# Optimization experiments

Measured on AMD Instinct MI355X. Metric: run time of the kernel, lower is better.

## Reference

```python
import jax, jax.numpy as jnp
import numpy as np

N, I, D, K = 64, 8192, 128, 16


def setup_inputs() -> dict:
    key = jax.random.key(0)
    k1, k2 = jax.random.split(key)
    x = jax.random.normal(k1, (N, I, D), dtype=jnp.float32)
    # each point belongs to one of k clusters of its own batch element -> offset n*K
    ci = jax.random.randint(k2, (N, I), 0, K) + jnp.arange(N)[:, None] * K
    return {
        "feature_matrix_batch": x,
        "cluster_index": ci.reshape(-1).astype(jnp.int32),  # [N*I]
        "k": K,
    }


def reference(feature_matrix_batch, cluster_index, k):
    n, i, d = feature_matrix_batch.shape
    flat = feature_matrix_batch.reshape(-1, d)  # [N*I, D]
    # scatter_max over segment ids -> [N*k, D]
    out = jax.ops.segment_max(flat, cluster_index, num_segments=n * k)
    return out.reshape(n, k, d)
```

## Files before the change

kernel.cpp:

```cpp
#include <hip/hip_runtime.h>
#include <stdint.h>

#define NB 64
#define NI 8192
#define ND 128
#define NK 16
#define SEG (NK * ND)
#define OUT_ELEMS (NB * SEG)
#define MAPPED_NEG_INF 0x007FFFFFu

typedef float f4 __attribute__((ext_vector_type(4)));
typedef uint32_t u4 __attribute__((ext_vector_type(4)));

__device__ __forceinline__ uint32_t map_f32(float f) {
    uint32_t b = __float_as_uint(f);
    return b ^ ((uint32_t)((int32_t)b >> 31) | 0x80000000u);
}
__device__ __forceinline__ uint32_t unmap_u32(uint32_t m) {
    return (m & 0x80000000u) ? (m ^ 0x80000000u) : ~m;
}

template <int PPB>
__global__ __launch_bounds__(256, 8) void seg_partial(
        const float* __restrict__ x,
        const int* __restrict__ ci,
        uint32_t* __restrict__ ws) {
    constexpr int BPB = NI / PPB;
    __shared__ uint32_t loc[SEG];
    __shared__ int cidx[PPB];

    const int t = threadIdx.x;
    const int b = blockIdx.x;
    const int batch = b / BPB;
    const int row0 = batch * NI + (b % BPB) * PPB;

    for (int i = t; i < SEG; i += 256) loc[i] = MAPPED_NEG_INF;
    if (t < PPB / 4) {
        int4 c = ((const int4*)(ci + row0))[t];
        const int base = batch * NK;
        c.x -= base; c.y -= base; c.z -= base; c.w -= base;
        ((int4*)cidx)[t] = c;
    }
    __syncthreads();

    const int lane32 = t & 31;
    const int rsub = t >> 5;
    const f4* xrow = (const f4*)(x + (size_t)row0 * ND) + lane32;

    #pragma unroll 2
    for (int it = 0; it < PPB / 8; ++it) {
        const int i = it * 8 + rsub;
        const int c = cidx[i];
        f4 v = __builtin_nontemporal_load(&xrow[(size_t)i * (ND / 4)]);
        uint32_t* lp = &loc[(c << 7) + lane32];
        atomicMax(&lp[0],  map_f32(v.x));
        atomicMax(&lp[32], map_f32(v.y));
        atomicMax(&lp[64], map_f32(v.z));
        atomicMax(&lp[96], map_f32(v.w));
    }
    __syncthreads();

    uint32_t* wb = ws + (size_t)b * SEG;
    for (int o = t; o < SEG; o += 256) {
        const int c = o >> 7;
        const int d = o & 127;
        wb[o] = loc[(c << 7) + ((d & 3) << 5) + (d >> 2)];
    }
}

template <int BPB>
__global__ __launch_bounds__(256) void seg_reduce(
        const uint32_t* __restrict__ ws,
        uint32_t* __restrict__ out) {
    const int idx = blockIdx.x * 256 + threadIdx.x;
    const int batch = idx >> 9;
    const int o4 = idx & (SEG / 4 - 1);
    const u4* p = (const u4*)(ws + (size_t)batch * BPB * SEG) + o4;
    u4 m;
    m.x = m.y = m.z = m.w = MAPPED_NEG_INF;
    #pragma unroll
    for (int j = 0; j < BPB; ++j) {
        u4 v = p[(size_t)j * (SEG / 4)];
        m.x = v.x > m.x ? v.x : m.x;
        m.y = v.y > m.y ? v.y : m.y;
        m.z = v.z > m.z ? v.z : m.z;
        m.w = v.w > m.w ? v.w : m.w;
    }
    u4 r;
    r.x = unmap_u32(m.x); r.y = unmap_u32(m.y);
    r.z = unmap_u32(m.z); r.w = unmap_u32(m.w);
    ((u4*)out)[idx] = r;
}

#define PPB_B 256
#define BPB_B (NI / PPB_B)

__global__ __launch_bounds__(256) void seg_init(uint32_t* __restrict__ out) {
    int idx = blockIdx.x * 256 + threadIdx.x;
    out[idx] = MAPPED_NEG_INF;
}

__global__ __launch_bounds__(256, 8) void seg_max_kernel(
        const float* __restrict__ x,
        const int* __restrict__ ci,
        uint32_t* __restrict__ out) {
    __shared__ uint32_t loc[SEG];
    __shared__ int cidx[PPB_B];

    const int t = threadIdx.x;
    const int b = blockIdx.x;
    const int batch = b >> 5;
    const int row0 = batch * NI + (b & (BPB_B - 1)) * PPB_B;

    for (int i = t; i < SEG; i += 256) loc[i] = MAPPED_NEG_INF;
    cidx[t] = ci[row0 + t] - batch * NK;
    __syncthreads();

    const int lane32 = t & 31;
    const int rsub = t >> 5;
    const f4* xrow = (const f4*)(x + (size_t)row0 * ND) + lane32;

    for (int it = 0; it < PPB_B / 8; ++it) {
        const int i = it * 8 + rsub;
        const int c = cidx[i];
        f4 v = xrow[(size_t)i * (ND / 4)];
        uint32_t* lp = &loc[(c << 7) + lane32];
        atomicMax(&lp[0],  map_f32(v.x));
        atomicMax(&lp[32], map_f32(v.y));
        atomicMax(&lp[64], map_f32(v.z));
        atomicMax(&lp[96], map_f32(v.w));
    }
    __syncthreads();

    uint32_t* ob = out + (size_t)batch * SEG;
    for (int o = t; o < SEG; o += 256) {
        const int c = o >> 7;
        const int d = o & 127;
        uint32_t v = loc[(c << 7) + ((d & 3) << 5) + (d >> 2)];
        if (v != MAPPED_NEG_INF) atomicMax(&ob[o], v);
    }
}

__global__ __launch_bounds__(256) void seg_decode(uint32_t* __restrict__ out) {
    int idx = blockIdx.x * 256 + threadIdx.x;
    out[idx] = unmap_u32(out[idx]);
}

extern "C" void kernel_launch(void* const* d_in, const int* in_sizes, int n_in,
                              void* d_out, int out_size, void* d_ws, size_t ws_size,
                              hipStream_t stream) {
    const float* x = (const float*)d_in[0];
    const int* ci = (const int*)d_in[1];
    uint32_t* out = (uint32_t*)d_out;

    const size_t ws_16mb = (size_t)2048 * SEG * 4;
    const size_t ws_8mb  = (size_t)1024 * SEG * 4;

    if (ws_size >= ws_16mb) {
        uint32_t* ws = (uint32_t*)d_ws;
        seg_partial<256><<<2048, 256, 0, stream>>>(x, ci, ws);
        seg_reduce<32><<<OUT_ELEMS / 4 / 256, 256, 0, stream>>>(ws, out);
    } else if (ws_size >= ws_8mb) {
        uint32_t* ws = (uint32_t*)d_ws;
        seg_partial<512><<<1024, 256, 0, stream>>>(x, ci, ws);
        seg_reduce<16><<<OUT_ELEMS / 4 / 256, 256, 0, stream>>>(ws, out);
    } else {
        seg_init<<<OUT_ELEMS / 256, 256, 0, stream>>>(out);
        seg_max_kernel<<<NB * BPB_B, 256, 0, stream>>>(x, ci, out);
        seg_decode<<<OUT_ELEMS / 256, 256, 0, stream>>>(out);
    }
}
```

Measured before the change: 55.27 us.

## Use 512-thread blocks over 1024 rows and vectorize workspace writes

The partial kernel now runs 512 threads per block over 1024 rows, giving 512 blocks instead of 2048. This cuts the workspace partials to 8 per batch and shrinks the reduce pass's reads. The workspace write-out now stores one 16-byte vector per thread, in a layout that maps directly to output order, instead of scalar transposed stores. The nontemporal load hint is dropped. Fewer blocks may reduce occupancy and latency hiding across the GPU's CUs.

```diff
diff --git a/kernel.cpp b/kernel.cpp
--- a/kernel.cpp
+++ b/kernel.cpp
@@ -8,6 +8,11 @@
 #define SEG (NK * ND)
 #define OUT_ELEMS (NB * SEG)
 #define MAPPED_NEG_INF 0x007FFFFFu
+
+#define PPB_A 1024
+#define BPB_A (NI / PPB_A)
+#define GRID_A (NB * BPB_A)
+#define WS_NEEDED ((size_t)GRID_A * SEG * 4)
 
 typedef float f4 __attribute__((ext_vector_type(4)));
 typedef uint32_t u4 __attribute__((ext_vector_type(4)));
@@ -20,22 +25,20 @@
     return (m & 0x80000000u) ? (m ^ 0x80000000u) : ~m;
 }
 
-template <int PPB>
-__global__ __launch_bounds__(256, 8) void seg_partial(
+__global__ __launch_bounds__(512, 4) void seg_partial(
         const float* __restrict__ x,
         const int* __restrict__ ci,
         uint32_t* __restrict__ ws) {
-    constexpr int BPB = NI / PPB;
     __shared__ uint32_t loc[SEG];
-    __shared__ int cidx[PPB];
+    __shared__ int cidx[PPB_A];
 
     const int t = threadIdx.x;
     const int b = blockIdx.x;
-    const int batch = b / BPB;
-    const int row0 = batch * NI + (b % BPB) * PPB;
+    const int batch = b >> 3;
+    const int row0 = batch * NI + (b & (BPB_A - 1)) * PPB_A;
 
-    for (int i = t; i < SEG; i += 256) loc[i] = MAPPED_NEG_INF;
-    if (t < PPB / 4) {
+    for (int i = t; i < SEG; i += 512) loc[i] = MAPPED_NEG_INF;
+    if (t < PPB_A / 4) {
         int4 c = ((const int4*)(ci + row0))[t];
         const int base = batch * NK;
         c.x -= base; c.y -= base; c.z -= base; c.w -= base;
@@ -48,10 +51,10 @@
     const f4* xrow = (const f4*)(x + (size_t)row0 * ND) + lane32;
 
     #pragma unroll 2
-    for (int it = 0; it < PPB / 8; ++it) {
-        const int i = it * 8 + rsub;
+    for (int it = 0; it < PPB_A / 16; ++it) {
+        const int i = it * 16 + rsub;
         const int c = cidx[i];
-        f4 v = __builtin_nontemporal_load(&xrow[(size_t)i * (ND / 4)]);
+        f4 v = xrow[(size_t)i * (ND / 4)];
         uint32_t* lp = &loc[(c << 7) + lane32];
         atomicMax(&lp[0],  map_f32(v.x));
         atomicMax(&lp[32], map_f32(v.y));
@@ -60,26 +63,29 @@
     }
     __syncthreads();
 
-    uint32_t* wb = ws + (size_t)b * SEG;
-    for (int o = t; o < SEG; o += 256) {
-        const int c = o >> 7;
-        const int d = o & 127;
-        wb[o] = loc[(c << 7) + ((d & 3) << 5) + (d >> 2)];
+    {
+        const int c = t >> 5;
+        const int dq = t & 31;
+        u4 r;
+        r.x = loc[(c << 7) + dq];
+        r.y = loc[(c << 7) + 32 + dq];
+        r.z = loc[(c << 7) + 64 + dq];
+        r.w = loc[(c << 7) + 96 + dq];
+        ((u4*)(ws + (size_t)b * SEG))[t] = r;
     }
 }
 
-template <int BPB>
 __global__ __launch_bounds__(256) void seg_reduce(
         const uint32_t* __restrict__ ws,
         uint32_t* __restrict__ out) {
     const int idx = blockIdx.x * 256 + threadIdx.x;
     const int batch = idx >> 9;
     const int o4 = idx & (SEG / 4 - 1);
-    const u4* p = (const u4*)(ws + (size_t)batch * BPB * SEG) + o4;
+    const u4* p = (const u4*)(ws + (size_t)batch * BPB_A * SEG) + o4;
     u4 m;
     m.x = m.y = m.z = m.w = MAPPED_NEG_INF;
     #pragma unroll
-    for (int j = 0; j < BPB; ++j) {
+    for (int j = 0; j < BPB_A; ++j) {
         u4 v = p[(size_t)j * (SEG / 4)];
         m.x = v.x > m.x ? v.x : m.x;
         m.y = v.y > m.y ? v.y : m.y;
@@ -153,17 +159,10 @@
     const int* ci = (const int*)d_in[1];
     uint32_t* out = (uint32_t*)d_out;
 
-    const size_t ws_16mb = (size_t)2048 * SEG * 4;
-    const size_t ws_8mb  = (size_t)1024 * SEG * 4;
-
-    if (ws_size >= ws_16mb) {
+    if (ws_size >= WS_NEEDED) {
         uint32_t* ws = (uint32_t*)d_ws;
-        seg_partial<256><<<2048, 256, 0, stream>>>(x, ci, ws);
-        seg_reduce<32><<<OUT_ELEMS / 4 / 256, 256, 0, stream>>>(ws, out);
-    } else if (ws_size >= ws_8mb) {
-        uint32_t* ws = (uint32_t*)d_ws;
-        seg_partial<512><<<1024, 256, 0, stream>>>(x, ci, ws);
-        seg_reduce<16><<<OUT_ELEMS / 4 / 256, 256, 0, stream>>>(ws, out);
+        seg_partial<<<GRID_A, 512, 0, stream>>>(x, ci, ws);
+        seg_reduce<<<OUT_ELEMS / 4 / 256, 256, 0, stream>>>(ws, out);
     } else {
         seg_init<<<OUT_ELEMS / 256, 256, 0, stream>>>(out);
         seg_max_kernel<<<NB * BPB_B, 256, 0, stream>>>(x, ci, out);
```

Result: faster. 50.00 us (-9.5%).
